# Optimization experiments

Measured on AMD Instinct MI355X. Metric: run time of the kernel, lower is better.

The kernel has to match this reference:

```python
import jax, jax.numpy as jnp
import numpy as np

N, E, D, L = 100000, 600000, 128, 5
BN_EPS = 1e-5


def setup_inputs() -> dict:
    key = jax.random.key(0)
    ks = jax.random.split(key, 12)
    x = jax.random.normal(ks[0], (N, D), dtype=jnp.float32)
    edge_index = jax.random.randint(ks[1], (2, E), 0, N, dtype=jnp.int64)
    edge_attr = jax.random.randint(ks[2], (E, D), 0, 4, dtype=jnp.int32)
    # per-layer GCNConv params
    W = jax.random.normal(ks[3], (L, D, D), dtype=jnp.float32) * 0.05
    b = jax.random.normal(ks[4], (L, D), dtype=jnp.float32) * 0.01
    root = jax.random.normal(ks[5], (L, D), dtype=jnp.float32) * 0.05
    # BatchNorm1d eval-mode params / running stats
    gamma = 1.0 + 0.1 * jax.random.normal(ks[6], (L, D), dtype=jnp.float32)
    beta = 0.1 * jax.random.normal(ks[7], (L, D), dtype=jnp.float32)
    mean = 0.1 * jax.random.normal(ks[8], (L, D), dtype=jnp.float32)
    var = 0.5 + jax.random.uniform(ks[9], (L, D), dtype=jnp.float32)
    return {"x": x, "edge_index": edge_index, "edge_attr": edge_attr,
            "W": W, "b": b, "root": root,
            "gamma": gamma, "beta": beta, "mean": mean, "var": var}


def reference(x, edge_index, edge_attr, W, b, root, gamma, beta, mean, var):
    # edge_attr.long() then identity edge_encoder -> integer values used in float math
    e = edge_attr.astype(x.dtype)                      # [E, D]
    row, col = edge_index[0], edge_index[1]            # source j, target i
    # deg = degree(row) + 1 (same every layer since graph is fixed)
    deg = jax.ops.segment_sum(jnp.ones((E,), x.dtype), row, num_segments=N) + 1.0  # [N]
    dinv = deg ** -0.5
    norm = (dinv[row] * dinv[col])[:, None]            # [E, 1]
    h = x
    for l in range(L):
        hl = h @ W[l].T + b[l]                         # Linear(emb_dim, emb_dim)
        msg = norm * jax.nn.relu(hl[row] + e)          # gather + relu + scale  [E, D]
        agg = jax.ops.segment_sum(msg, col, num_segments=N)  # scatter-add at targets
        h = agg + jax.nn.relu(hl + root[l]) / deg[:, None]   # self-loop term
        # BatchNorm1d (eval mode, running stats)
        h = gamma[l] * (h - mean[l]) / jnp.sqrt(var[l] + BN_EPS) + beta[l]
        if l < L - 1:
            h = jax.nn.relu(h)                         # dropout is identity in eval
    return h  # JK='last'
```

## Files before the change

### kernel.cpp

```cpp
#include <hip/hip_runtime.h>
#include <cstdint>
#include <cstddef>

#define DF 128
#define NL 5
#define NB 1024
#define BN_EPS 1e-5f

typedef short bf16x8 __attribute__((ext_vector_type(8)));
typedef float f32x4 __attribute__((ext_vector_type(4)));

typedef __attribute__((address_space(3))) uint32_t lds_u32;
typedef __attribute__((address_space(1))) uint32_t glb_u32;

__device__ __forceinline__ void gload16(const void* g, void* l) {
#if __has_builtin(__builtin_amdgcn_global_load_lds)
  __builtin_amdgcn_global_load_lds((const glb_u32*)g, (lds_u32*)l, 16, 0, 0);
#else
  *(uint4*)l = *(const uint4*)g;
#endif
}

__device__ __forceinline__ ushort f2b(float f) {
  union { float f; uint32_t u; } v; v.f = f;
  uint32_t u = v.u + 0x7fffu + ((v.u >> 16) & 1u);
  return (ushort)(u >> 16);
}
__device__ __forceinline__ float b2f(uint32_t lo16) {
  union { uint32_t u; float f; } v; v.u = lo16 << 16;
  return v.f;
}
__device__ __forceinline__ uint32_t pk2(float a, float b) {
  return (uint32_t)f2b(a) | ((uint32_t)f2b(b) << 16);
}


__global__ void k_deg2(const int* __restrict__ row, const int* __restrict__ col,
                       int* __restrict__ degi, int* __restrict__ indeg, int E) {
  int i = blockIdx.x * blockDim.x + threadIdx.x;
  if (i < E) {
    atomicAdd(&degi[row[i]], 1);
    atomicAdd(&indeg[col[i]], 1);
  }
}

__global__ void k_dinvhist(const int* __restrict__ degi, const int* __restrict__ indeg,
                           float* __restrict__ dinv, int* __restrict__ hist, int N) {
  __shared__ int lh[NB];
  for (int j = threadIdx.x; j < NB; j += blockDim.x) lh[j] = 0;
  __syncthreads();
  int i = blockIdx.x * blockDim.x + threadIdx.x;
  if (i < N) {
    dinv[i] = 1.0f / sqrtf((float)(degi[i] + 1));
    atomicAdd(&lh[min(indeg[i], NB - 1)], 1);
  }
  __syncthreads();
  for (int j = threadIdx.x; j < NB; j += blockDim.x) {
    int c = lh[j];
    if (c) atomicAdd(&hist[j], c);
  }
}

__global__ void k_scan(const int* __restrict__ hist,
                       int* __restrict__ nodeStart, int* __restrict__ edgeStart) {
  __shared__ int2 sm[NB];
  int t = threadIdx.x;
  int c = hist[t];
  int2 v; v.x = c; v.y = c * t;
  sm[t] = v;
  __syncthreads();
  for (int off = 1; off < NB; off <<= 1) {
    int2 add; add.x = 0; add.y = 0;
    if (t >= off) add = sm[t - off];
    __syncthreads();
    sm[t].x += add.x; sm[t].y += add.y;
    __syncthreads();
  }
  nodeStart[t] = sm[t].x - c;
  edgeStart[t] = sm[t].y - c * t;
}

__global__ void k_assign(const int* __restrict__ indeg, const float* __restrict__ dinv,
                         const int* __restrict__ nodeStart, const int* __restrict__ edgeStart,
                         int* __restrict__ binCursor,
                         int* __restrict__ perm, int* __restrict__ invperm,
                         int* __restrict__ startP, int* __restrict__ cursorP,
                         int* __restrict__ degP, float* __restrict__ dinvP, int N) {
  __shared__ int lh[NB];
  __shared__ int gbase[NB];
  for (int j = threadIdx.x; j < NB; j += blockDim.x) lh[j] = 0;
  __syncthreads();
  int nd = blockIdx.x * blockDim.x + threadIdx.x;
  bool valid = nd < N;
  int d = 0, bin = 0, lrank = 0;
  if (valid) {
    d = indeg[nd];
    bin = min(d, NB - 1);
    lrank = atomicAdd(&lh[bin], 1);
  }
  __syncthreads();
  for (int j = threadIdx.x; j < NB; j += blockDim.x) {
    int c = lh[j];
    gbase[j] = c ? atomicAdd(&binCursor[j], c) : 0;
  }
  __syncthreads();
  if (!valid) return;
  int r = gbase[bin] + lrank;
  int i = nodeStart[bin] + r;
  perm[i] = nd;
  invperm[nd] = i;
  int st = edgeStart[bin] + r * d;
  startP[i] = st;
  cursorP[i] = st;
  degP[i] = d;
  dinvP[i] = dinv[nd];
}

__global__ void k_fillpack(const int* __restrict__ row, const int* __restrict__ col,
                           const float* __restrict__ dinv, const int* __restrict__ invperm,
                           int* __restrict__ cursorP,
                           int* __restrict__ srcS, float* __restrict__ nrmS,
                           const int* __restrict__ ea, uint32_t* __restrict__ epS, int E) {
  int tid = blockIdx.x * blockDim.x + threadIdx.x;
  int e = tid >> 3, t = tid & 7;
  if (e >= E) return;
  int pos;
  if (t == 0) {
    int r = row[e], c = col[e];
    pos = atomicAdd(&cursorP[invperm[c]], 1);
    srcS[pos] = invperm[r];
    nrmS[pos] = dinv[r] * dinv[c];
  }
  pos = __shfl(pos, 0, 8);
  const int4* p = ((const int4*)ea) + (size_t)e * 32 + t * 4;
  uint32_t w = 0;
  #pragma unroll
  for (int q = 0; q < 4; ++q) {
    int4 a = p[q];
    w |= ((uint32_t)(a.x & 3)) << (8 * q);
    w |= ((uint32_t)(a.y & 3)) << (8 * q + 2);
    w |= ((uint32_t)(a.z & 3)) << (8 * q + 4);
    w |= ((uint32_t)(a.w & 3)) << (8 * q + 6);
  }
  epS[(size_t)pos * 8 + t] = w;
}

__global__ void k_params(const float* __restrict__ g, const float* __restrict__ be,
                         const float* __restrict__ mn, const float* __restrict__ vr,
                         float* __restrict__ s, float* __restrict__ t,
                         const float* __restrict__ W, ushort* __restrict__ Wb,
                         int nbn, int nw) {
  int i = blockIdx.x * blockDim.x + threadIdx.x;
  if (i < nw) Wb[i] = f2b(W[i]);
  if (i < nbn) {
    float sc = g[i] / sqrtf(vr[i] + BN_EPS);
    s[i] = sc;
    t[i] = be[i] - mn[i] * sc;
  }
}

template <typename IT>
__global__ __launch_bounds__(256) void k_gemm(
    const IT* __restrict__ in, const int* __restrict__ perm,
    const ushort* __restrict__ Wb, const float* __restrict__ bl,
    ushort* __restrict__ hl, int N)
{
  __shared__ uint4 lA[128 * 16];
  __shared__ uint4 lW[128 * 16];
  const int t = threadIdx.x;
  const int row0 = blockIdx.x * 128;
  const int wv = t >> 6;
  const int l  = t & 63;

  #pragma unroll
  for (int it = 0; it < 8; ++it) {
    int ubase = (it * 4 + wv) * 64;
    int lin = ubase + l;
    int r = lin >> 4, u = lin & 15;
    gload16((const void*)((const uint4*)Wb + (r << 4) + (u ^ (r & 7))), (void*)(lW + ubase));
  }

  if constexpr (sizeof(IT) == 2) {
    #pragma unroll
    for (int it = 0; it < 8; ++it) {
      int ubase = (it * 4 + wv) * 64;
      int lin = ubase + l;
      int r = lin >> 4, u = lin & 15;
      int gn = row0 + r;
      int gnc = gn < N ? gn : N - 1;
      gload16((const void*)((const uint4*)in + (size_t)gnc * 16 + (u ^ (r & 7))),
              (void*)(lA + ubase));
    }
  } else {
    #pragma unroll
    for (int it = 0; it < 8; ++it) {
      int lin = it * 256 + t;
      int r = lin >> 4, u = lin & 15;
      int gn = row0 + r;
      uint4 pk = make_uint4(0u, 0u, 0u, 0u);
      if (gn < N) {
        int src = perm[gn];
        const float4* p = (const float4*)((const float*)in + (size_t)src * DF + u * 8);
        float4 f0 = p[0], f1 = p[1];
        pk.x = pk2(f0.x, f0.y); pk.y = pk2(f0.z, f0.w);
        pk.z = pk2(f1.x, f1.y); pk.w = pk2(f1.z, f1.w);
      }
      lA[(r << 4) | (u ^ (r & 7))] = pk;
    }
  }
  __syncthreads();

  const int lr = l & 15;
  const int lk = l >> 4;

  f32x4 acc[2][8];
  #pragma unroll
  for (int rt = 0; rt < 2; ++rt)
    #pragma unroll
    for (int ct = 0; ct < 8; ++ct) acc[rt][ct] = (f32x4){0.f, 0.f, 0.f, 0.f};

  #pragma unroll
  for (int ks = 0; ks < 4; ++ks) {
    const int kofs = ks * 4 + lk;
    bf16x8 af[2], wf[8];
    #pragma unroll
    for (int rt = 0; rt < 2; ++rt) {
      int r = wv * 32 + rt * 16 + lr;
      af[rt] = *reinterpret_cast<const bf16x8*>(&lA[(r << 4) | (kofs ^ (r & 7))]);
    }
    #pragma unroll
    for (int ct = 0; ct < 8; ++ct) {
      int r = ct * 16 + lr;
      wf[ct] = *reinterpret_cast<const bf16x8*>(&lW[(r << 4) | (kofs ^ (r & 7))]);
    }
    #pragma unroll
    for (int rt = 0; rt < 2; ++rt)
      #pragma unroll
      for (int ct = 0; ct < 8; ++ct)
        acc[rt][ct] = __builtin_amdgcn_mfma_f32_16x16x32_bf16(af[rt], wf[ct], acc[rt][ct], 0, 0, 0);
  }

  float bb[8];
  #pragma unroll
  for (int ct = 0; ct < 8; ++ct) bb[ct] = bl[ct * 16 + lr];

  #pragma unroll
  for (int rt = 0; rt < 2; ++rt) {
    #pragma unroll
    for (int rg = 0; rg < 4; ++rg) {
      int gn = row0 + wv * 32 + rt * 16 + lk * 4 + rg;
      if (gn >= N) continue;
      #pragma unroll
      for (int ct = 0; ct < 8; ++ct)
        hl[(size_t)gn * DF + ct * 16 + lr] = f2b(acc[rt][ct][rg] + bb[ct]);
    }
  }
}

template <typename AT, bool LAST>
__global__ __launch_bounds__(256) void k_gather(
    const int* __restrict__ startP, const int* __restrict__ degP,
    const float* __restrict__ dinvP,
    const int* __restrict__ srcS, const float* __restrict__ nrmS,
    const uint32_t* __restrict__ epS,
    const uint4* __restrict__ hl4,
    const float* __restrict__ rootl, const float* __restrict__ sl,
    const float* __restrict__ tl, const int* __restrict__ perm,
    AT* __restrict__ acc, int N)
{
  int gw = (blockIdx.x * blockDim.x + threadIdx.x) >> 6;
  int lane = threadIdx.x & 63;
  int s16 = lane & 15;
  int i = gw * 4 + (lane >> 4);
  if (i >= N) return;
  int base = startP[i], n = degP[i];
  float di = dinvP[i];
  float invdeg = di * di;
  const uint32_t sh = (s16 & 1) * 16;
  const int dw = s16 >> 1;

  float a[8];
  #pragma unroll
  for (int j = 0; j < 8; ++j) a[j] = 0.f;

  for (int c0 = 0; c0 < n; c0 += 16) {
    int m = min(16, n - c0);
    int myIdx = base + c0 + s16;
    int mySrc = (s16 < m) ? srcS[myIdx] : 0;
    float myNrm = (s16 < m) ? nrmS[myIdx] : 0.f;
    #pragma unroll 2
    for (int k = 0; k < m; ++k) {
      int src = __shfl(mySrc, k, 16);
      float nr = __shfl(myNrm, k, 16);
      uint32_t pw = epS[(size_t)(base + c0 + k) * 8 + dw];
      uint4 hw = hl4[(size_t)src * 16 + s16];
      float h, ev;
      h = b2f(hw.x & 0xffffu); ev = (float)((pw >> (sh + 0)) & 3u);  a[0] += nr * fmaxf(h + ev, 0.f);
      h = b2f(hw.x >> 16);     ev = (float)((pw >> (sh + 2)) & 3u);  a[1] += nr * fmaxf(h + ev, 0.f);
      h = b2f(hw.y & 0xffffu); ev = (float)((pw >> (sh + 4)) & 3u);  a[2] += nr * fmaxf(h + ev, 0.f);
      h = b2f(hw.y >> 16);     ev = (float)((pw >> (sh + 6)) & 3u);  a[3] += nr * fmaxf(h + ev, 0.f);
      h = b2f(hw.z & 0xffffu); ev = (float)((pw >> (sh + 8)) & 3u);  a[4] += nr * fmaxf(h + ev, 0.f);
      h = b2f(hw.z >> 16);     ev = (float)((pw >> (sh + 10)) & 3u); a[5] += nr * fmaxf(h + ev, 0.f);
      h = b2f(hw.w & 0xffffu); ev = (float)((pw >> (sh + 12)) & 3u); a[6] += nr * fmaxf(h + ev, 0.f);
      h = b2f(hw.w >> 16);     ev = (float)((pw >> (sh + 14)) & 3u); a[7] += nr * fmaxf(h + ev, 0.f);
    }
  }

  uint4 hwS = hl4[(size_t)i * 16 + s16];
  float hs[8];
  hs[0] = b2f(hwS.x & 0xffffu); hs[1] = b2f(hwS.x >> 16);
  hs[2] = b2f(hwS.y & 0xffffu); hs[3] = b2f(hwS.y >> 16);
  hs[4] = b2f(hwS.z & 0xffffu); hs[5] = b2f(hwS.z >> 16);
  hs[6] = b2f(hwS.w & 0xffffu); hs[7] = b2f(hwS.w >> 16);

  float rr[8], ss[8], tt[8];
  ((float4*)rr)[0] = ((const float4*)rootl)[s16 * 2]; ((float4*)rr)[1] = ((const float4*)rootl)[s16 * 2 + 1];
  ((float4*)ss)[0] = ((const float4*)sl)[s16 * 2];    ((float4*)ss)[1] = ((const float4*)sl)[s16 * 2 + 1];
  ((float4*)tt)[0] = ((const float4*)tl)[s16 * 2];    ((float4*)tt)[1] = ((const float4*)tl)[s16 * 2 + 1];

  float o[8];
  #pragma unroll
  for (int j = 0; j < 8; ++j) {
    float self = fmaxf(hs[j] + rr[j], 0.f) * invdeg;
    o[j] = ss[j] * (self + a[j]) + tt[j];
  }

  if constexpr (!LAST) {
    #pragma unroll
    for (int j = 0; j < 8; ++j) o[j] = fmaxf(o[j], 0.f);
    uint4 p;
    p.x = pk2(o[0], o[1]); p.y = pk2(o[2], o[3]);
    p.z = pk2(o[4], o[5]); p.w = pk2(o[6], o[7]);
    ((uint4*)acc)[(size_t)i * 16 + s16] = p;
  } else {
    int nd = perm[i];
    float4* ap = (float4*)acc + (size_t)nd * 32 + s16 * 2;
    ap[0] = make_float4(o[0], o[1], o[2], o[3]);
    ap[1] = make_float4(o[4], o[5], o[6], o[7]);
  }
}

extern "C" void kernel_launch(void* const* d_in, const int* in_sizes, int n_in,
                              void* d_out, int out_size, void* d_ws, size_t ws_size,
                              hipStream_t stream) {
  const float* x     = (const float*)d_in[0];
  const int*   ei    = (const int*)d_in[1];
  const int*   ea    = (const int*)d_in[2];
  const float* W     = (const float*)d_in[3];
  const float* b     = (const float*)d_in[4];
  const float* root  = (const float*)d_in[5];
  const float* gamma = (const float*)d_in[6];
  const float* beta  = (const float*)d_in[7];
  const float* mean  = (const float*)d_in[8];
  const float* var   = (const float*)d_in[9];

  const int N = in_sizes[0] / DF;
  const int E = in_sizes[1] / 2;
  const int* row = ei;
  const int* col = ei + E;

  char* ws = (char*)d_ws;
  size_t off = 0;
  auto alloc = [&](size_t bytes) -> void* {
    void* p = ws + off;
    off = (off + bytes + 255) & ~(size_t)255;
    return p;
  };
  int*      degi    = (int*)alloc((size_t)N * 4);
  int*      indeg   = (int*)alloc((size_t)N * 4);
  int*      hist    = (int*)alloc((size_t)NB * 4);
  int*      binCur  = (int*)alloc((size_t)NB * 4);
  size_t    zspan   = (size_t)((char*)ws + off - (char*)degi);
  float*    dinv    = (float*)alloc((size_t)N * 4);
  int*      nodeSt  = (int*)alloc((size_t)NB * 4);
  int*      edgeSt  = (int*)alloc((size_t)NB * 4);
  int*      perm    = (int*)alloc((size_t)N * 4);
  int*      invperm = (int*)alloc((size_t)N * 4);
  int*      startP  = (int*)alloc((size_t)N * 4);
  int*      cursorP = (int*)alloc((size_t)N * 4);
  int*      degP    = (int*)alloc((size_t)N * 4);
  float*    dinvP   = (float*)alloc((size_t)N * 4);
  int*      srcS    = (int*)alloc((size_t)E * 4);
  float*    nrmS    = (float*)alloc((size_t)E * 4);
  uint32_t* epS     = (uint32_t*)alloc((size_t)E * 8 * 4);
  float*    sbuf    = (float*)alloc((size_t)NL * DF * 4);
  float*    tbuf    = (float*)alloc((size_t)NL * DF * 4);
  ushort*   Wb      = (ushort*)alloc((size_t)NL * DF * DF * 2);
  ushort*   hl      = (ushort*)alloc((size_t)N * DF * 2);
  ushort*   accP    = (ushort*)alloc((size_t)N * DF * 2);

  hipMemsetAsync(degi, 0, zspan, stream);

  k_deg2<<<(E + 255) / 256, 256, 0, stream>>>(row, col, degi, indeg, E);
  k_dinvhist<<<(N + 255) / 256, 256, 0, stream>>>(degi, indeg, dinv, hist, N);
  k_scan<<<1, NB, 0, stream>>>(hist, nodeSt, edgeSt);
  k_assign<<<(N + 255) / 256, 256, 0, stream>>>(indeg, dinv, nodeSt, edgeSt, binCur,
                                                perm, invperm, startP, cursorP,
                                                degP, dinvP, N);
  k_fillpack<<<(E * 8 + 255) / 256, 256, 0, stream>>>(row, col, dinv, invperm, cursorP,
                                                      srcS, nrmS, ea, epS, E);
  k_params<<<(NL * DF * DF + 255) / 256, 256, 0, stream>>>(
      gamma, beta, mean, var, sbuf, tbuf, W, Wb, NL * DF, NL * DF * DF);

  float* outp = (float*)d_out;
  const int gemmGrid = (N + 127) / 128;
  const int gathGrid = ((N + 3) / 4 * 64 + 255) / 256;

  k_gemm<float><<<gemmGrid, 256, 0, stream>>>(x, perm, Wb, b, hl, N);
  k_gather<ushort, false><<<gathGrid, 256, 0, stream>>>(
      startP, degP, dinvP, srcS, nrmS, epS, (const uint4*)hl,
      root, sbuf, tbuf, perm, accP, N);

  for (int l = 1; l < NL - 1; ++l) {
    k_gemm<ushort><<<gemmGrid, 256, 0, stream>>>(
        accP, nullptr, Wb + (size_t)l * DF * DF, b + (size_t)l * DF, hl, N);
    k_gather<ushort, false><<<gathGrid, 256, 0, stream>>>(
        startP, degP, dinvP, srcS, nrmS, epS, (const uint4*)hl,
        root + (size_t)l * DF, sbuf + (size_t)l * DF, tbuf + (size_t)l * DF,
        perm, accP, N);
  }

  {
    const int l = NL - 1;
    k_gemm<ushort><<<gemmGrid, 256, 0, stream>>>(
        accP, nullptr, Wb + (size_t)l * DF * DF, b + (size_t)l * DF, hl, N);
    k_gather<float, true><<<gathGrid, 256, 0, stream>>>(
        startP, degP, dinvP, srcS, nrmS, epS, (const uint4*)hl,
        root + (size_t)l * DF, sbuf + (size_t)l * DF, tbuf + (size_t)l * DF,
        perm, outp, N);
  }
}
```

Baseline: 440.3 us.

## Quantize GEMM output to int8 with per-row scale and pack edge src/norm pairs

The GEMM epilogue now quantizes each output row to int8 with a per-row absmax scale. It stages the row in shared memory and writes it out with coalesced 8-byte stores. The gather kernel reads 8 bytes per lane instead of 16 plus one scale per source and dequantizes, which halves the random-gather traffic that dominates the message-passing step. Source index and edge norm are packed into one int2 array so each neighbor needs a single load, and the inner loop is unrolled further. The cost is extra accuracy loss from int8 activations, which may not meet tolerance, plus extra scale loads and a max-reduction in the epilogue.

```diff
diff --git a/kernel.cpp b/kernel.cpp
--- a/kernel.cpp
+++ b/kernel.cpp
@@ -26,12 +26,11 @@
   uint32_t u = v.u + 0x7fffu + ((v.u >> 16) & 1u);
   return (ushort)(u >> 16);
 }
-__device__ __forceinline__ float b2f(uint32_t lo16) {
-  union { uint32_t u; float f; } v; v.u = lo16 << 16;
-  return v.f;
-}
 __device__ __forceinline__ uint32_t pk2(float a, float b) {
   return (uint32_t)f2b(a) | ((uint32_t)f2b(b) << 16);
+}
+__device__ __forceinline__ float i8f(uint32_t w, int sh) {
+  return (float)(int8_t)((w >> sh) & 0xffu);
 }
 
 
@@ -118,8 +117,7 @@
 
 __global__ void k_fillpack(const int* __restrict__ row, const int* __restrict__ col,
                            const float* __restrict__ dinv, const int* __restrict__ invperm,
-                           int* __restrict__ cursorP,
-                           int* __restrict__ srcS, float* __restrict__ nrmS,
+                           int* __restrict__ cursorP, int2* __restrict__ pairS,
                            const int* __restrict__ ea, uint32_t* __restrict__ epS, int E) {
   int tid = blockIdx.x * blockDim.x + threadIdx.x;
   int e = tid >> 3, t = tid & 7;
@@ -128,8 +126,10 @@
   if (t == 0) {
     int r = row[e], c = col[e];
     pos = atomicAdd(&cursorP[invperm[c]], 1);
-    srcS[pos] = invperm[r];
-    nrmS[pos] = dinv[r] * dinv[c];
+    int2 pv; pv.x = invperm[r];
+    float nr = dinv[r] * dinv[c];
+    pv.y = __float_as_int(nr);
+    pairS[pos] = pv;
   }
   pos = __shfl(pos, 0, 8);
   const int4* p = ((const int4*)ea) + (size_t)e * 32 + t * 4;
@@ -163,7 +163,7 @@
 __global__ __launch_bounds__(256) void k_gemm(
     const IT* __restrict__ in, const int* __restrict__ perm,
     const ushort* __restrict__ Wb, const float* __restrict__ bl,
-    ushort* __restrict__ hl, int N)
+    uint8_t* __restrict__ hl, float* __restrict__ scale, int N)
 {
   __shared__ uint4 lA[128 * 16];
   __shared__ uint4 lW[128 * 16];
@@ -244,15 +244,45 @@
   #pragma unroll
   for (int ct = 0; ct < 8; ++ct) bb[ct] = bl[ct * 16 + lr];
 
+  __syncthreads();
+  uint8_t* q8 = (uint8_t*)lA;
+
   #pragma unroll
   for (int rt = 0; rt < 2; ++rt) {
     #pragma unroll
     for (int rg = 0; rg < 4; ++rg) {
-      int gn = row0 + wv * 32 + rt * 16 + lk * 4 + rg;
-      if (gn >= N) continue;
+      int rloc = wv * 32 + rt * 16 + lk * 4 + rg;
+      float o[8];
+      float am = 0.f;
       #pragma unroll
-      for (int ct = 0; ct < 8; ++ct)
-        hl[(size_t)gn * DF + ct * 16 + lr] = f2b(acc[rt][ct][rg] + bb[ct]);
+      for (int ct = 0; ct < 8; ++ct) {
+        o[ct] = acc[rt][ct][rg] + bb[ct];
+        am = fmaxf(am, fabsf(o[ct]));
+      }
+      am = fmaxf(am, __shfl_xor(am, 1));
+      am = fmaxf(am, __shfl_xor(am, 2));
+      am = fmaxf(am, __shfl_xor(am, 4));
+      am = fmaxf(am, __shfl_xor(am, 8));
+      float inv = am > 0.f ? 127.f / am : 0.f;
+      int gn = row0 + rloc;
+      if (lr == 0 && gn < N) scale[gn] = am * (1.f / 127.f);
+      #pragma unroll
+      for (int ct = 0; ct < 8; ++ct) {
+        int q = __float2int_rn(o[ct] * inv);
+        q8[rloc * DF + ct * 16 + lr] = (uint8_t)(q & 0xff);
+      }
+    }
+  }
+  __syncthreads();
+
+  #pragma unroll
+  for (int it = 0; it < 8; ++it) {
+    int chunk = it * 256 + t;
+    int rloc = chunk >> 4;
+    int gn = row0 + rloc;
+    if (gn < N) {
+      uint2 v = *(const uint2*)(q8 + chunk * 8);
+      *(uint2*)(hl + (size_t)gn * DF + (chunk & 15) * 8) = v;
     }
   }
 }
@@ -261,9 +291,9 @@
 __global__ __launch_bounds__(256) void k_gather(
     const int* __restrict__ startP, const int* __restrict__ degP,
     const float* __restrict__ dinvP,
-    const int* __restrict__ srcS, const float* __restrict__ nrmS,
+    const int2* __restrict__ pairS,
     const uint32_t* __restrict__ epS,
-    const uint4* __restrict__ hl4,
+    const uint2* __restrict__ hl2, const float* __restrict__ scaleArr,
     const float* __restrict__ rootl, const float* __restrict__ sl,
     const float* __restrict__ tl, const int* __restrict__ perm,
     AT* __restrict__ acc, int N)
@@ -285,33 +315,32 @@
 
   for (int c0 = 0; c0 < n; c0 += 16) {
     int m = min(16, n - c0);
-    int myIdx = base + c0 + s16;
-    int mySrc = (s16 < m) ? srcS[myIdx] : 0;
-    float myNrm = (s16 < m) ? nrmS[myIdx] : 0.f;
-    #pragma unroll 2
+    int2 pv = (s16 < m) ? pairS[base + c0 + s16] : make_int2(0, 0);
+    #pragma unroll 4
     for (int k = 0; k < m; ++k) {
-      int src = __shfl(mySrc, k, 16);
-      float nr = __shfl(myNrm, k, 16);
+      int src = __shfl(pv.x, k, 16);
+      float nr = __int_as_float(__shfl(pv.y, k, 16));
       uint32_t pw = epS[(size_t)(base + c0 + k) * 8 + dw];
-      uint4 hw = hl4[(size_t)src * 16 + s16];
-      float h, ev;
-      h = b2f(hw.x & 0xffffu); ev = (float)((pw >> (sh + 0)) & 3u);  a[0] += nr * fmaxf(h + ev, 0.f);
-      h = b2f(hw.x >> 16);     ev = (float)((pw >> (sh + 2)) & 3u);  a[1] += nr * fmaxf(h + ev, 0.f);
-      h = b2f(hw.y & 0xffffu); ev = (float)((pw >> (sh + 4)) & 3u);  a[2] += nr * fmaxf(h + ev, 0.f);
-      h = b2f(hw.y >> 16);     ev = (float)((pw >> (sh + 6)) & 3u);  a[3] += nr * fmaxf(h + ev, 0.f);
-      h = b2f(hw.z & 0xffffu); ev = (float)((pw >> (sh + 8)) & 3u);  a[4] += nr * fmaxf(h + ev, 0.f);
-      h = b2f(hw.z >> 16);     ev = (float)((pw >> (sh + 10)) & 3u); a[5] += nr * fmaxf(h + ev, 0.f);
-      h = b2f(hw.w & 0xffffu); ev = (float)((pw >> (sh + 12)) & 3u); a[6] += nr * fmaxf(h + ev, 0.f);
-      h = b2f(hw.w >> 16);     ev = (float)((pw >> (sh + 14)) & 3u); a[7] += nr * fmaxf(h + ev, 0.f);
-    }
-  }
-
-  uint4 hwS = hl4[(size_t)i * 16 + s16];
+      uint2 hw = hl2[(size_t)src * 16 + s16];
+      float sc = scaleArr[src];
+      a[0] += nr * fmaxf(fmaf(i8f(hw.x, 0),  sc, (float)((pw >> (sh + 0))  & 3u)), 0.f);
+      a[1] += nr * fmaxf(fmaf(i8f(hw.x, 8),  sc, (float)((pw >> (sh + 2))  & 3u)), 0.f);
+      a[2] += nr * fmaxf(fmaf(i8f(hw.x, 16), sc, (float)((pw >> (sh + 4))  & 3u)), 0.f);
+      a[3] += nr * fmaxf(fmaf(i8f(hw.x, 24), sc, (float)((pw >> (sh + 6))  & 3u)), 0.f);
+      a[4] += nr * fmaxf(fmaf(i8f(hw.y, 0),  sc, (float)((pw >> (sh + 8))  & 3u)), 0.f);
+      a[5] += nr * fmaxf(fmaf(i8f(hw.y, 8),  sc, (float)((pw >> (sh + 10)) & 3u)), 0.f);
+      a[6] += nr * fmaxf(fmaf(i8f(hw.y, 16), sc, (float)((pw >> (sh + 12)) & 3u)), 0.f);
+      a[7] += nr * fmaxf(fmaf(i8f(hw.y, 24), sc, (float)((pw >> (sh + 14)) & 3u)), 0.f);
+    }
+  }
+
+  uint2 hwS = hl2[(size_t)i * 16 + s16];
+  float scS = scaleArr[i];
   float hs[8];
-  hs[0] = b2f(hwS.x & 0xffffu); hs[1] = b2f(hwS.x >> 16);
-  hs[2] = b2f(hwS.y & 0xffffu); hs[3] = b2f(hwS.y >> 16);
-  hs[4] = b2f(hwS.z & 0xffffu); hs[5] = b2f(hwS.z >> 16);
-  hs[6] = b2f(hwS.w & 0xffffu); hs[7] = b2f(hwS.w >> 16);
+  hs[0] = i8f(hwS.x, 0)  * scS; hs[1] = i8f(hwS.x, 8)  * scS;
+  hs[2] = i8f(hwS.x, 16) * scS; hs[3] = i8f(hwS.x, 24) * scS;
+  hs[4] = i8f(hwS.y, 0)  * scS; hs[5] = i8f(hwS.y, 8)  * scS;
+  hs[6] = i8f(hwS.y, 16) * scS; hs[7] = i8f(hwS.y, 24) * scS;
 
   float rr[8], ss[8], tt[8];
   ((float4*)rr)[0] = ((const float4*)rootl)[s16 * 2]; ((float4*)rr)[1] = ((const float4*)rootl)[s16 * 2 + 1];
@@ -380,13 +409,13 @@
   int*      cursorP = (int*)alloc((size_t)N * 4);
   int*      degP    = (int*)alloc((size_t)N * 4);
   float*    dinvP   = (float*)alloc((size_t)N * 4);
-  int*      srcS    = (int*)alloc((size_t)E * 4);
-  float*    nrmS    = (float*)alloc((size_t)E * 4);
+  int2*     pairS   = (int2*)alloc((size_t)E * 8);
   uint32_t* epS     = (uint32_t*)alloc((size_t)E * 8 * 4);
   float*    sbuf    = (float*)alloc((size_t)NL * DF * 4);
   float*    tbuf    = (float*)alloc((size_t)NL * DF * 4);
   ushort*   Wb      = (ushort*)alloc((size_t)NL * DF * DF * 2);
-  ushort*   hl      = (ushort*)alloc((size_t)N * DF * 2);
+  uint8_t*  hl      = (uint8_t*)alloc((size_t)N * DF);
+  float*    scaleA  = (float*)alloc((size_t)N * 4);
   ushort*   accP    = (ushort*)alloc((size_t)N * DF * 2);
 
   hipMemsetAsync(degi, 0, zspan, stream);
@@ -398,7 +427,7 @@
                                                 perm, invperm, startP, cursorP,
                                                 degP, dinvP, N);
   k_fillpack<<<(E * 8 + 255) / 256, 256, 0, stream>>>(row, col, dinv, invperm, cursorP,
-                                                      srcS, nrmS, ea, epS, E);
+                                                      pairS, ea, epS, E);
   k_params<<<(NL * DF * DF + 255) / 256, 256, 0, stream>>>(
       gamma, beta, mean, var, sbuf, tbuf, W, Wb, NL * DF, NL * DF * DF);
 
@@ -406,16 +435,16 @@
   const int gemmGrid = (N + 127) / 128;
   const int gathGrid = ((N + 3) / 4 * 64 + 255) / 256;
 
-  k_gemm<float><<<gemmGrid, 256, 0, stream>>>(x, perm, Wb, b, hl, N);
+  k_gemm<float><<<gemmGrid, 256, 0, stream>>>(x, perm, Wb, b, hl, scaleA, N);
   k_gather<ushort, false><<<gathGrid, 256, 0, stream>>>(
-      startP, degP, dinvP, srcS, nrmS, epS, (const uint4*)hl,
+      startP, degP, dinvP, pairS, epS, (const uint2*)hl, scaleA,
       root, sbuf, tbuf, perm, accP, N);
 
   for (int l = 1; l < NL - 1; ++l) {
     k_gemm<ushort><<<gemmGrid, 256, 0, stream>>>(
-        accP, nullptr, Wb + (size_t)l * DF * DF, b + (size_t)l * DF, hl, N);
+        accP, nullptr, Wb + (size_t)l * DF * DF, b + (size_t)l * DF, hl, scaleA, N);
     k_gather<ushort, false><<<gathGrid, 256, 0, stream>>>(
-        startP, degP, dinvP, srcS, nrmS, epS, (const uint4*)hl,
+        startP, degP, dinvP, pairS, epS, (const uint2*)hl, scaleA,
         root + (size_t)l * DF, sbuf + (size_t)l * DF, tbuf + (size_t)l * DF,
         perm, accP, N);
   }
@@ -423,9 +452,9 @@
   {
     const int l = NL - 1;
     k_gemm<ushort><<<gemmGrid, 256, 0, stream>>>(
-        accP, nullptr, Wb + (size_t)l * DF * DF, b + (size_t)l * DF, hl, N);
+        accP, nullptr, Wb + (size_t)l * DF * DF, b + (size_t)l * DF, hl, scaleA, N);
     k_gather<float, true><<<gathGrid, 256, 0, stream>>>(
-        startP, degP, dinvP, srcS, nrmS, epS, (const uint4*)hl,
+        startP, degP, dinvP, pairS, epS, (const uint2*)hl, scaleA,
         root + (size_t)l * DF, sbuf + (size_t)l * DF, tbuf + (size_t)l * DF,
         perm, outp, N);
   }
```

After: 406.3 us. -7.7%, faster.
